# Performance work log

Hardware: AMD Instinct MI355X
Metric: run time of the kernel (lower is better)

## Reference

```python
import jax, jax.numpy as jnp
import numpy as np

B, C, F = 8, 2048, 128


def setup_inputs() -> dict:
    key = jax.random.key(0)
    ks = jax.random.split(key, 13)
    features = jax.random.normal(ks[0], (B, C, F), dtype=jnp.float32)
    # sparse-ish boolean adjacency masks over operations
    pred_mask = jax.random.uniform(ks[1], (B, C, C)) < 0.05
    succ_mask = jax.random.uniform(ks[2], (B, C, C)) < 0.05
    same_type_mask = jax.random.uniform(ks[3], (B, C, C)) < 0.10

    def linear(k, fan_in, fan_out):
        kw, kb = jax.random.split(k)
        bound = 1.0 / np.sqrt(fan_in)
        W = jax.random.uniform(kw, (fan_in, fan_out), minval=-bound, maxval=bound, dtype=jnp.float32)
        b = jax.random.uniform(kb, (fan_out,), minval=-bound, maxval=bound, dtype=jnp.float32)
        return W, b

    W_enc, b_enc = linear(ks[4], F, 4 * F)
    W_space, b_space = linear(ks[5], 3 * F, F)
    W_same, b_same = linear(ks[6], 2 * F, F)
    W_mix, b_mix = linear(ks[7], 2 * F, F)
    return {
        "features": features,
        "pred_mask": pred_mask,
        "succ_mask": succ_mask,
        "same_type_mask": same_type_mask,
        "W_enc": W_enc, "b_enc": b_enc,
        "W_space": W_space, "b_space": b_space,
        "W_same": W_same, "b_same": b_same,
        "W_mix": W_mix, "b_mix": b_mix,
    }


def reference(features, pred_mask, succ_mask, same_type_mask,
              W_enc, b_enc, W_space, b_space, W_same, b_same, W_mix, b_mix):
    # encoder: [B,C,F] -> [B,C,4F], split into origin + 3 message features
    enc = features @ W_enc + b_enc
    origin, e_pred, e_succ, e_same = jnp.split(enc, 4, axis=-1)

    def masked_mean(mask, e):
        # original builds (B,C,C,F) broadcast product then sums over 'other';
        # mathematically this is mask @ e with a clamped-degree divisor.
        m = mask.astype(e.dtype)                         # [B,C,C]
        deg = jnp.maximum(m.sum(-1, keepdims=True), 1.0)  # [B,C,1]
        return jnp.einsum('bij,bjf->bif', m, e) / deg

    pred_f = masked_mean(pred_mask, e_pred)
    succ_f = masked_mean(succ_mask, e_succ)
    same_f = masked_mean(same_type_mask, e_same)

    space_mixed = jnp.concatenate([pred_f, origin, succ_f], axis=-1) @ W_space + b_space
    same_mixed = jnp.concatenate([origin, same_f], axis=-1) @ W_same + b_same
    return jnp.concatenate([space_mixed, same_mixed], axis=-1) @ W_mix + b_mix
```

## Files before the change

kernel.cpp:

```cpp
#include <hip/hip_runtime.h>
#include <stdint.h>

typedef unsigned int uint;
typedef unsigned short ushort;
typedef unsigned char uchar;
typedef __attribute__((ext_vector_type(8))) short bf16x8;
typedef __attribute__((ext_vector_type(4))) float f32x4;

__device__ __forceinline__ ushort f2bf(float f) {
  uint u = __builtin_bit_cast(uint, f);
  return (ushort)((u + 0x7FFFu + ((u >> 16) & 1u)) >> 16);
}

__global__ __launch_bounds__(256) void k_detect(
    const uint* __restrict__ m, int* __restrict__ esz_out) {
  __shared__ int s_ok;
  if (threadIdx.x == 0) s_ok = 1;
  __syncthreads();
  int ok = 1;
  for (int i = 0; i < 64; ++i) {
    uint v = m[(size_t)threadIdx.x * 64 + i];
    if (!(v == 0u || v == 1u || v == 0x3F800000u)) ok = 0;
  }
  if (!ok) atomicAnd(&s_ok, 0);
  __syncthreads();
  if (threadIdx.x == 0) *esz_out = s_ok ? 4 : 1;
}

__global__ __launch_bounds__(256) void k_cvt_feat(
    const float4* __restrict__ in, ushort* __restrict__ out) {
  for (int i = blockIdx.x * 256 + threadIdx.x; i < 524288; i += 65536) {
    float4 v = in[i];
    ushort4 o;
    o.x = f2bf(v.x); o.y = f2bf(v.y); o.z = f2bf(v.z); o.w = f2bf(v.w);
    *(ushort4*)&out[(size_t)i * 4] = o;
  }
}

__global__ __launch_bounds__(256) void k_twt(
    const float* __restrict__ We, const float* __restrict__ Ws,
    const float* __restrict__ Wm, const float* __restrict__ Wx,
    ushort* __restrict__ Te, ushort* __restrict__ Ts,
    ushort* __restrict__ Tm, ushort* __restrict__ Tx) {
  int i = blockIdx.x * 256 + threadIdx.x;
  if (i < 65536) { int n = i >> 7, k = i & 127; Te[i] = f2bf(We[k * 512 + n]); return; }
  i -= 65536;
  if (i < 49152) { int n = i / 384, k = i - n * 384; Ts[i] = f2bf(Ws[k * 128 + n]); return; }
  i -= 49152;
  if (i < 32768) { int n = i >> 8, k = i & 255; Tm[i] = f2bf(Wm[k * 128 + n]); return; }
  i -= 32768;
  if (i < 32768) { int n = i >> 8, k = i & 255; Tx[i] = f2bf(Wx[k * 128 + n]); return; }
}

__device__ __forceinline__ void mfma_tiles(const ushort* As, const ushort* Bs,
                                           int m0w, int n0w, int lr, int quad,
                                           f32x4 acc[2][4]) {
#pragma unroll
  for (int kc = 0; kc < 2; ++kc) {
    bf16x8 a[2], b[4];
#pragma unroll
    for (int i = 0; i < 2; ++i)
      a[i] = *(const bf16x8*)&As[(m0w + i * 16 + lr) * 72 + kc * 32 + quad * 8];
#pragma unroll
    for (int j = 0; j < 4; ++j)
      b[j] = *(const bf16x8*)&Bs[(n0w + j * 16 + lr) * 72 + kc * 32 + quad * 8];
#pragma unroll
    for (int i = 0; i < 2; ++i)
#pragma unroll
      for (int j = 0; j < 4; ++j)
        acc[i][j] = __builtin_amdgcn_mfma_f32_16x16x32_bf16(a[i], b[j], acc[i][j], 0, 0, 0);
  }
}

__global__ __launch_bounds__(256) void k_enc(
    const ushort* __restrict__ featbf, const ushort* __restrict__ WTe,
    const float* __restrict__ bias, ushort* __restrict__ origin,
    ushort* __restrict__ eT0, ushort* __restrict__ eT1, ushort* __restrict__ eT2) {
  __shared__ ushort As[64 * 72];
  __shared__ ushort Bs[128 * 72];
  const int t = threadIdx.x;
  const int gm0 = blockIdx.x * 64;
  const int y = blockIdx.y;
  const ushort* Bsrc = WTe + (size_t)y * 128 * 128;
  const int lane = t & 63, wave = t >> 6;
  const int m0w = (wave >> 1) * 32, n0w = (wave & 1) * 64;
  const int quad = lane >> 4, lr = lane & 15;
  const int am = t >> 2, aq = t & 3;
  const int bn = t >> 1, bh = t & 1;
  f32x4 acc[2][4] = {};
  for (int k0 = 0; k0 < 128; k0 += 64) {
    const ushort* asrc = featbf + (size_t)(gm0 + am) * 128 + k0 + aq * 16;
    bf16x8 av0 = *(const bf16x8*)asrc;
    bf16x8 av1 = *(const bf16x8*)(asrc + 8);
    const ushort* bsrc = Bsrc + (size_t)bn * 128 + k0 + bh * 32;
    bf16x8 bv0 = *(const bf16x8*)bsrc;
    bf16x8 bv1 = *(const bf16x8*)(bsrc + 8);
    bf16x8 bv2 = *(const bf16x8*)(bsrc + 16);
    bf16x8 bv3 = *(const bf16x8*)(bsrc + 24);
    *(bf16x8*)&As[am * 72 + aq * 16] = av0;
    *(bf16x8*)&As[am * 72 + aq * 16 + 8] = av1;
    *(bf16x8*)&Bs[bn * 72 + bh * 32] = bv0;
    *(bf16x8*)&Bs[bn * 72 + bh * 32 + 8] = bv1;
    *(bf16x8*)&Bs[bn * 72 + bh * 32 + 16] = bv2;
    *(bf16x8*)&Bs[bn * 72 + bh * 32 + 24] = bv3;
    __syncthreads();
    mfma_tiles(As, Bs, m0w, n0w, lr, quad, acc);
    __syncthreads();
  }
  ushort* eT = (y == 1) ? eT0 : (y == 2) ? eT1 : eT2;
#pragma unroll
  for (int i = 0; i < 2; ++i)
#pragma unroll
    for (int j = 0; j < 4; ++j)
#pragma unroll
      for (int r = 0; r < 4; ++r) {
        int m = gm0 + m0w + i * 16 + quad * 4 + r;
        int n = n0w + j * 16 + lr;
        ushort h = f2bf(acc[i][j][r] + bias[y * 128 + n]);
        if (y == 0) origin[(size_t)m * 128 + n] = h;
        else eT[(size_t)n * 16384 + m] = h;
      }
}

__global__ __launch_bounds__(256) void k_mm(
    const void* __restrict__ mp, const void* __restrict__ ms, const void* __restrict__ mt,
    const ushort* __restrict__ eT0, const ushort* __restrict__ eT1, const ushort* __restrict__ eT2,
    ushort* __restrict__ P, ushort* __restrict__ S, ushort* __restrict__ T,
    const int* __restrict__ esz_p) {
  __shared__ ushort As[64 * 72];
  __shared__ ushort Bs[128 * 72];
  __shared__ uint degs[64];
  const int t = threadIdx.x;
  const int mtile = blockIdx.x, b = blockIdx.y, mid = blockIdx.z;
  const void* mask = (mid == 0) ? mp : (mid == 1) ? ms : mt;
  const ushort* eT = (mid == 0) ? eT0 : (mid == 1) ? eT1 : eT2;
  ushort* outp = (mid == 0) ? P : (mid == 1) ? S : T;
  const int esz = *esz_p;
  if (t < 64) degs[t] = 0;
  const size_t rowbase = (size_t)b * 2048 + mtile * 64;
  const int lane = t & 63, wave = t >> 6;
  const int m0w = (wave >> 1) * 32, n0w = (wave & 1) * 64;
  const int quad = lane >> 4, lr = lane & 15;
  const int am = t >> 2, aq = t & 3;
  const int bn = t >> 1, bh = t & 1;
  const ushort* bsrc_base = eT + (size_t)bn * 16384 + (size_t)b * 2048 + bh * 32;
  f32x4 acc[2][4] = {};
  int cnt = 0;
  for (int k0 = 0; k0 < 2048; k0 += 64) {
    bf16x8 o0, o1;
    if (esz == 4) {
      const uint* p = (const uint*)mask + (rowbase + am) * 2048 + k0 + aq * 16;
      uint w[16];
      *(uint4*)&w[0] = *(const uint4*)p;
      *(uint4*)&w[4] = *(const uint4*)(p + 4);
      *(uint4*)&w[8] = *(const uint4*)(p + 8);
      *(uint4*)&w[12] = *(const uint4*)(p + 12);
#pragma unroll
      for (int e = 0; e < 8; ++e) { int nz = (w[e] != 0u); o0[e] = nz ? (short)0x3F80 : (short)0; cnt += nz; }
#pragma unroll
      for (int e = 0; e < 8; ++e) { int nz = (w[e + 8] != 0u); o1[e] = nz ? (short)0x3F80 : (short)0; cnt += nz; }
    } else {
      const uchar* p = (const uchar*)mask + (rowbase + am) * 2048 + k0 + aq * 16;
      uint4 wb = *(const uint4*)p;
      uint arr[4] = {wb.x, wb.y, wb.z, wb.w};
#pragma unroll
      for (int e = 0; e < 8; ++e) { int nz = (((arr[e >> 2] >> ((e & 3) * 8)) & 0xFFu) != 0u); o0[e] = nz ? (short)0x3F80 : (short)0; cnt += nz; }
#pragma unroll
      for (int e = 0; e < 8; ++e) { int ee = e + 8; int nz = (((arr[ee >> 2] >> ((ee & 3) * 8)) & 0xFFu) != 0u); o1[e] = nz ? (short)0x3F80 : (short)0; cnt += nz; }
    }
    const ushort* bsrc = bsrc_base + k0;
    bf16x8 bv0 = *(const bf16x8*)bsrc;
    bf16x8 bv1 = *(const bf16x8*)(bsrc + 8);
    bf16x8 bv2 = *(const bf16x8*)(bsrc + 16);
    bf16x8 bv3 = *(const bf16x8*)(bsrc + 24);
    *(bf16x8*)&As[am * 72 + aq * 16] = o0;
    *(bf16x8*)&As[am * 72 + aq * 16 + 8] = o1;
    *(bf16x8*)&Bs[bn * 72 + bh * 32] = bv0;
    *(bf16x8*)&Bs[bn * 72 + bh * 32 + 8] = bv1;
    *(bf16x8*)&Bs[bn * 72 + bh * 32 + 16] = bv2;
    *(bf16x8*)&Bs[bn * 72 + bh * 32 + 24] = bv3;
    __syncthreads();
    mfma_tiles(As, Bs, m0w, n0w, lr, quad, acc);
    __syncthreads();
  }
  atomicAdd(&degs[am], (uint)cnt);
  __syncthreads();
#pragma unroll
  for (int i = 0; i < 2; ++i)
#pragma unroll
    for (int r = 0; r < 4; ++r) {
      int ml = m0w + i * 16 + quad * 4 + r;
      uint d = degs[ml];
      float inv = 1.0f / (float)(d > 0u ? d : 1u);
#pragma unroll
      for (int j = 0; j < 4; ++j) {
        int n = n0w + j * 16 + lr;
        outp[(rowbase + ml) * 128 + n] = f2bf(acc[i][j][r] * inv);
      }
    }
}

__global__ __launch_bounds__(256) void k_gemm(
    const ushort* __restrict__ A0, const ushort* __restrict__ A1,
    const ushort* __restrict__ A2, const ushort* __restrict__ Bsrc,
    int bstride, int K, const float* __restrict__ bias,
    void* __restrict__ out, int out_f32) {
  __shared__ ushort As[64 * 72];
  __shared__ ushort Bs[128 * 72];
  const int t = threadIdx.x;
  const int gm0 = blockIdx.x * 64;
  const int lane = t & 63, wave = t >> 6;
  const int m0w = (wave >> 1) * 32, n0w = (wave & 1) * 64;
  const int quad = lane >> 4, lr = lane & 15;
  const int am = t >> 2, aq = t & 3;
  const int bn = t >> 1, bh = t & 1;
  f32x4 acc[2][4] = {};
  for (int k0 = 0; k0 < K; k0 += 64) {
    const int seg = k0 >> 7;
    const ushort* Ap = (seg == 0) ? A0 : (seg == 1) ? A1 : A2;
    const ushort* asrc = Ap + (size_t)(gm0 + am) * 128 + (k0 & 127) + aq * 16;
    bf16x8 av0 = *(const bf16x8*)asrc;
    bf16x8 av1 = *(const bf16x8*)(asrc + 8);
    const ushort* bsrc = Bsrc + (size_t)bn * bstride + k0 + bh * 32;
    bf16x8 bv0 = *(const bf16x8*)bsrc;
    bf16x8 bv1 = *(const bf16x8*)(bsrc + 8);
    bf16x8 bv2 = *(const bf16x8*)(bsrc + 16);
    bf16x8 bv3 = *(const bf16x8*)(bsrc + 24);
    *(bf16x8*)&As[am * 72 + aq * 16] = av0;
    *(bf16x8*)&As[am * 72 + aq * 16 + 8] = av1;
    *(bf16x8*)&Bs[bn * 72 + bh * 32] = bv0;
    *(bf16x8*)&Bs[bn * 72 + bh * 32 + 8] = bv1;
    *(bf16x8*)&Bs[bn * 72 + bh * 32 + 16] = bv2;
    *(bf16x8*)&Bs[bn * 72 + bh * 32 + 24] = bv3;
    __syncthreads();
    mfma_tiles(As, Bs, m0w, n0w, lr, quad, acc);
    __syncthreads();
  }
#pragma unroll
  for (int i = 0; i < 2; ++i)
#pragma unroll
    for (int j = 0; j < 4; ++j)
#pragma unroll
      for (int r = 0; r < 4; ++r) {
        int m = gm0 + m0w + i * 16 + quad * 4 + r;
        int n = n0w + j * 16 + lr;
        float v = acc[i][j][r] + bias[n];
        if (out_f32) ((float*)out)[(size_t)m * 128 + n] = v;
        else ((ushort*)out)[(size_t)m * 128 + n] = f2bf(v);
      }
}

extern "C" void kernel_launch(void* const* d_in, const int* in_sizes, int n_in,
                              void* d_out, int out_size, void* d_ws,
                              size_t ws_size, hipStream_t stream) {
  const float* features = (const float*)d_in[0];
  const void* pred = d_in[1];
  const void* succ = d_in[2];
  const void* same = d_in[3];
  const float* W_enc = (const float*)d_in[4];
  const float* b_enc = (const float*)d_in[5];
  const float* W_space = (const float*)d_in[6];
  const float* b_space = (const float*)d_in[7];
  const float* W_same = (const float*)d_in[8];
  const float* b_same = (const float*)d_in[9];
  const float* W_mix = (const float*)d_in[10];
  const float* b_mix = (const float*)d_in[11];

  const size_t M = 16384;
  ushort* w = (ushort*)d_ws;
  ushort* feat_bf = w;  w += M * 128;
  ushort* WT_enc = w;   w += 512 * 128;
  ushort* WT_space = w; w += 128 * 384;
  ushort* WT_same = w;  w += 128 * 256;
  ushort* WT_mix = w;   w += 128 * 256;
  ushort* origin = w;   w += M * 128;
  ushort* eT0 = w;      w += M * 128;
  ushort* eT1 = w;      w += M * 128;
  ushort* eT2 = w;      w += M * 128;
  ushort* P = w;        w += M * 128;
  ushort* S = w;        w += M * 128;
  ushort* T = w;        w += M * 128;
  ushort* X = w;        w += M * 128;
  ushort* Y = w;        w += M * 128;
  int* esz = (int*)w;

  k_detect<<<1, 256, 0, stream>>>((const uint*)pred, esz);
  k_cvt_feat<<<256, 256, 0, stream>>>((const float4*)features, feat_bf);
  k_twt<<<704, 256, 0, stream>>>(W_enc, W_space, W_same, W_mix,
                                 WT_enc, WT_space, WT_same, WT_mix);
  k_enc<<<dim3(256, 4), 256, 0, stream>>>(feat_bf, WT_enc, b_enc,
                                          origin, eT0, eT1, eT2);
  k_mm<<<dim3(32, 8, 3), 256, 0, stream>>>(pred, succ, same, eT0, eT1, eT2,
                                           P, S, T, esz);
  k_gemm<<<256, 256, 0, stream>>>(P, origin, S, WT_space, 384, 384,
                                  b_space, X, 0);
  k_gemm<<<256, 256, 0, stream>>>(origin, T, nullptr, WT_same, 256, 256,
                                  b_same, Y, 0);
  k_gemm<<<256, 256, 0, stream>>>(X, Y, nullptr, WT_mix, 256, 256,
                                  b_mix, d_out, 1);
}
```

Baseline: 452.6 us.

## Fold linear layers into encoder weights and fuse mask-matmul with output accumulation

Uses linearity to precompose the space/same/mix weights with the encoder weights on device, so each adjacency term becomes mask @ (features @ U) and the three trailing GEMMs disappear. The per-row bias contributions are folded into constant vectors, applied only when a row's degree is nonzero. The mask kernel now loads masks directly into registers with double buffering instead of staging through LDS, reads pre-swizzled eT tiles written via an LDS stage in the encoder, remaps blocks across XCDs, and accumulates into the fp32 output with atomics. Feature conversion is folded into the encoder and mask-format detection samples across all three masks. The float atomics make the summation order nondeterministic, and composing the weights before rounding to bf16 changes the numerics.

```diff
diff --git a/kernel.cpp b/kernel.cpp
--- a/kernel.cpp
+++ b/kernel.cpp
@@ -13,75 +13,81 @@
 }
 
 __global__ __launch_bounds__(256) void k_detect(
-    const uint* __restrict__ m, int* __restrict__ esz_out) {
-  __shared__ int s_ok;
-  if (threadIdx.x == 0) s_ok = 1;
-  __syncthreads();
-  int ok = 1;
-  for (int i = 0; i < 64; ++i) {
-    uint v = m[(size_t)threadIdx.x * 64 + i];
-    if (!(v == 0u || v == 1u || v == 0x3F800000u)) ok = 0;
-  }
-  if (!ok) atomicAnd(&s_ok, 0);
-  __syncthreads();
-  if (threadIdx.x == 0) *esz_out = s_ok ? 4 : 1;
-}
-
-__global__ __launch_bounds__(256) void k_cvt_feat(
-    const float4* __restrict__ in, ushort* __restrict__ out) {
-  for (int i = blockIdx.x * 256 + threadIdx.x; i < 524288; i += 65536) {
-    float4 v = in[i];
-    ushort4 o;
-    o.x = f2bf(v.x); o.y = f2bf(v.y); o.z = f2bf(v.z); o.w = f2bf(v.w);
-    *(ushort4*)&out[(size_t)i * 4] = o;
-  }
-}
-
-__global__ __launch_bounds__(256) void k_twt(
-    const float* __restrict__ We, const float* __restrict__ Ws,
-    const float* __restrict__ Wm, const float* __restrict__ Wx,
-    ushort* __restrict__ Te, ushort* __restrict__ Ts,
-    ushort* __restrict__ Tm, ushort* __restrict__ Tx) {
-  int i = blockIdx.x * 256 + threadIdx.x;
-  if (i < 65536) { int n = i >> 7, k = i & 127; Te[i] = f2bf(We[k * 512 + n]); return; }
-  i -= 65536;
-  if (i < 49152) { int n = i / 384, k = i - n * 384; Ts[i] = f2bf(Ws[k * 128 + n]); return; }
-  i -= 49152;
-  if (i < 32768) { int n = i >> 8, k = i & 255; Tm[i] = f2bf(Wm[k * 128 + n]); return; }
-  i -= 32768;
-  if (i < 32768) { int n = i >> 8, k = i & 255; Tx[i] = f2bf(Wx[k * 128 + n]); return; }
-}
-
-__device__ __forceinline__ void mfma_tiles(const ushort* As, const ushort* Bs,
-                                           int m0w, int n0w, int lr, int quad,
-                                           f32x4 acc[2][4]) {
-#pragma unroll
-  for (int kc = 0; kc < 2; ++kc) {
-    bf16x8 a[2], b[4];
-#pragma unroll
-    for (int i = 0; i < 2; ++i)
-      a[i] = *(const bf16x8*)&As[(m0w + i * 16 + lr) * 72 + kc * 32 + quad * 8];
-#pragma unroll
-    for (int j = 0; j < 4; ++j)
-      b[j] = *(const bf16x8*)&Bs[(n0w + j * 16 + lr) * 72 + kc * 32 + quad * 8];
-#pragma unroll
-    for (int i = 0; i < 2; ++i)
-#pragma unroll
-      for (int j = 0; j < 4; ++j)
-        acc[i][j] = __builtin_amdgcn_mfma_f32_16x16x32_bf16(a[i], b[j], acc[i][j], 0, 0, 0);
+    const uint* __restrict__ mp, const uint* __restrict__ ms,
+    const uint* __restrict__ mt, int* __restrict__ esz) {
+  int bid = blockIdx.x;
+  const uint* m = (bid < 64) ? mp : (bid < 128) ? ms : mt;
+  uint v = m[(size_t)(bid & 63) * 65521 + threadIdx.x];
+  if (!(v == 0u || v == 1u || v == 0x3F800000u)) atomicAnd(esz, 0);
+}
+
+__global__ __launch_bounds__(256) void k_fuse1(
+    const float* __restrict__ Ws, const float* __restrict__ Wsame,
+    const float* __restrict__ Wm, float* __restrict__ T1, float* __restrict__ T2) {
+  int idx = blockIdx.x * 256 + threadIdx.x;
+  if (idx >= 81920) return;
+  int r = idx >> 7, n = idx & 127;
+  float s = 0.f;
+  if (r < 384) {
+    for (int c = 0; c < 128; ++c) s += Ws[r * 128 + c] * Wm[c * 128 + n];
+    T1[r * 128 + n] = s;
+  } else {
+    int rr = r - 384;
+    for (int c = 0; c < 128; ++c) s += Wsame[rr * 128 + c] * Wm[(128 + c) * 128 + n];
+    T2[rr * 128 + n] = s;
+  }
+}
+
+__global__ __launch_bounds__(256) void k_fuse2(
+    const float* __restrict__ We, const float* __restrict__ be,
+    const float* __restrict__ bs, const float* __restrict__ bsame,
+    const float* __restrict__ bm, const float* __restrict__ Wm,
+    const float* __restrict__ T1, const float* __restrict__ T2,
+    ushort* __restrict__ UT, float* __restrict__ cvec) {
+  int idx = blockIdx.x * 256 + threadIdx.x;
+  if (idx < 65536) {
+    int y = idx >> 14, n = (idx >> 7) & 127, k = idx & 127;
+    float s = 0.f;
+    if (y == 0)
+      for (int m = 0; m < 128; ++m)
+        s += We[k * 512 + m] * (T1[(128 + m) * 128 + n] + T2[m * 128 + n]);
+    else if (y == 1)
+      for (int m = 0; m < 128; ++m) s += We[k * 512 + 128 + m] * T1[m * 128 + n];
+    else if (y == 2)
+      for (int m = 0; m < 128; ++m) s += We[k * 512 + 256 + m] * T1[(256 + m) * 128 + n];
+    else
+      for (int m = 0; m < 128; ++m) s += We[k * 512 + 384 + m] * T2[(128 + m) * 128 + n];
+    UT[((size_t)y * 128 + n) * 128 + k] = f2bf(s);
+  } else if (idx < 66048) {
+    int cid = idx - 65536, cv = cid >> 7, n = cid & 127;
+    float s = 0.f;
+    if (cv == 0) {
+      for (int m = 0; m < 128; ++m)
+        s += be[m] * (T1[(128 + m) * 128 + n] + T2[m * 128 + n]);
+      for (int c = 0; c < 128; ++c) s += bs[c] * Wm[c * 128 + n];
+      for (int c = 0; c < 128; ++c) s += bsame[c] * Wm[(128 + c) * 128 + n];
+      s += bm[n];
+    } else if (cv == 1) {
+      for (int m = 0; m < 128; ++m) s += be[128 + m] * T1[m * 128 + n];
+    } else if (cv == 2) {
+      for (int m = 0; m < 128; ++m) s += be[256 + m] * T1[(256 + m) * 128 + n];
+    } else {
+      for (int m = 0; m < 128; ++m) s += be[384 + m] * T2[(128 + m) * 128 + n];
+    }
+    cvec[cv * 128 + n] = s;
   }
 }
 
 __global__ __launch_bounds__(256) void k_enc(
-    const ushort* __restrict__ featbf, const ushort* __restrict__ WTe,
-    const float* __restrict__ bias, ushort* __restrict__ origin,
+    const float* __restrict__ feat, const ushort* __restrict__ UT,
+    const float* __restrict__ cvec, float* __restrict__ out,
     ushort* __restrict__ eT0, ushort* __restrict__ eT1, ushort* __restrict__ eT2) {
   __shared__ ushort As[64 * 72];
   __shared__ ushort Bs[128 * 72];
+  __shared__ ushort stage[8192];
   const int t = threadIdx.x;
   const int gm0 = blockIdx.x * 64;
   const int y = blockIdx.y;
-  const ushort* Bsrc = WTe + (size_t)y * 128 * 128;
   const int lane = t & 63, wave = t >> 6;
   const int m0w = (wave >> 1) * 32, n0w = (wave & 1) * 64;
   const int quad = lane >> 4, lr = lane & 15;
@@ -89,102 +95,187 @@
   const int bn = t >> 1, bh = t & 1;
   f32x4 acc[2][4] = {};
   for (int k0 = 0; k0 < 128; k0 += 64) {
-    const ushort* asrc = featbf + (size_t)(gm0 + am) * 128 + k0 + aq * 16;
-    bf16x8 av0 = *(const bf16x8*)asrc;
-    bf16x8 av1 = *(const bf16x8*)(asrc + 8);
-    const ushort* bsrc = Bsrc + (size_t)bn * 128 + k0 + bh * 32;
+    const float* asrc = feat + (size_t)(gm0 + am) * 128 + k0 + aq * 16;
+    float4 f0 = *(const float4*)asrc;
+    float4 f1 = *(const float4*)(asrc + 4);
+    float4 f2 = *(const float4*)(asrc + 8);
+    float4 f3 = *(const float4*)(asrc + 12);
+    ushort h[16];
+    h[0] = f2bf(f0.x); h[1] = f2bf(f0.y); h[2] = f2bf(f0.z); h[3] = f2bf(f0.w);
+    h[4] = f2bf(f1.x); h[5] = f2bf(f1.y); h[6] = f2bf(f1.z); h[7] = f2bf(f1.w);
+    h[8] = f2bf(f2.x); h[9] = f2bf(f2.y); h[10] = f2bf(f2.z); h[11] = f2bf(f2.w);
+    h[12] = f2bf(f3.x); h[13] = f2bf(f3.y); h[14] = f2bf(f3.z); h[15] = f2bf(f3.w);
+    const ushort* bsrc = UT + ((size_t)y * 128 + bn) * 128 + k0 + bh * 32;
     bf16x8 bv0 = *(const bf16x8*)bsrc;
     bf16x8 bv1 = *(const bf16x8*)(bsrc + 8);
     bf16x8 bv2 = *(const bf16x8*)(bsrc + 16);
     bf16x8 bv3 = *(const bf16x8*)(bsrc + 24);
-    *(bf16x8*)&As[am * 72 + aq * 16] = av0;
-    *(bf16x8*)&As[am * 72 + aq * 16 + 8] = av1;
+    *(bf16x8*)&As[am * 72 + aq * 16] = *(bf16x8*)&h[0];
+    *(bf16x8*)&As[am * 72 + aq * 16 + 8] = *(bf16x8*)&h[8];
     *(bf16x8*)&Bs[bn * 72 + bh * 32] = bv0;
     *(bf16x8*)&Bs[bn * 72 + bh * 32 + 8] = bv1;
     *(bf16x8*)&Bs[bn * 72 + bh * 32 + 16] = bv2;
     *(bf16x8*)&Bs[bn * 72 + bh * 32 + 24] = bv3;
     __syncthreads();
-    mfma_tiles(As, Bs, m0w, n0w, lr, quad, acc);
+#pragma unroll
+    for (int kc = 0; kc < 2; ++kc) {
+      bf16x8 a[2], b[4];
+#pragma unroll
+      for (int i = 0; i < 2; ++i)
+        a[i] = *(const bf16x8*)&As[(m0w + i * 16 + lr) * 72 + kc * 32 + quad * 8];
+#pragma unroll
+      for (int j = 0; j < 4; ++j)
+        b[j] = *(const bf16x8*)&Bs[(n0w + j * 16 + lr) * 72 + kc * 32 + quad * 8];
+#pragma unroll
+      for (int i = 0; i < 2; ++i)
+#pragma unroll
+        for (int j = 0; j < 4; ++j)
+          acc[i][j] = __builtin_amdgcn_mfma_f32_16x16x32_bf16(a[i], b[j], acc[i][j], 0, 0, 0);
+    }
     __syncthreads();
   }
-  ushort* eT = (y == 1) ? eT0 : (y == 2) ? eT1 : eT2;
-#pragma unroll
-  for (int i = 0; i < 2; ++i)
-#pragma unroll
-    for (int j = 0; j < 4; ++j)
-#pragma unroll
-      for (int r = 0; r < 4; ++r) {
-        int m = gm0 + m0w + i * 16 + quad * 4 + r;
-        int n = n0w + j * 16 + lr;
-        ushort h = f2bf(acc[i][j][r] + bias[y * 128 + n]);
-        if (y == 0) origin[(size_t)m * 128 + n] = h;
-        else eT[(size_t)n * 16384 + m] = h;
-      }
-}
-
-__global__ __launch_bounds__(256) void k_mm(
-    const void* __restrict__ mp, const void* __restrict__ ms, const void* __restrict__ mt,
-    const ushort* __restrict__ eT0, const ushort* __restrict__ eT1, const ushort* __restrict__ eT2,
-    ushort* __restrict__ P, ushort* __restrict__ S, ushort* __restrict__ T,
+  if (y == 0) {
+#pragma unroll
+    for (int i = 0; i < 2; ++i)
+#pragma unroll
+      for (int j = 0; j < 4; ++j)
+#pragma unroll
+        for (int r = 0; r < 4; ++r) {
+          int m = gm0 + m0w + i * 16 + quad * 4 + r;
+          int n = n0w + j * 16 + lr;
+          out[(size_t)m * 128 + n] = acc[i][j][r] + cvec[n];
+        }
+  } else {
+#pragma unroll
+    for (int i = 0; i < 2; ++i)
+#pragma unroll
+      for (int j = 0; j < 4; ++j)
+#pragma unroll
+        for (int r = 0; r < 4; ++r) {
+          int rl = m0w + i * 16 + quad * 4 + r;
+          int n = n0w + j * 16 + lr;
+          int kc = rl >> 5, qd = (rl >> 3) & 3, e = rl & 7;
+          stage[((((n >> 4) * 2 + kc) * 4 + qd) * 16 + (n & 15)) * 8 + e] =
+              f2bf(acc[i][j][r]);
+        }
+    __syncthreads();
+    ushort* eT = (y == 1) ? eT0 : (y == 2) ? eT1 : eT2;
+    ushort* dst = eT + ((size_t)(gm0 >> 11) * 32 + ((gm0 >> 6) & 31)) * 8192 + t * 32;
+    const ushort* src = stage + t * 32;
+#pragma unroll
+    for (int p = 0; p < 4; ++p)
+      *(bf16x8*)(dst + p * 8) = *(const bf16x8*)(src + p * 8);
+  }
+}
+
+__global__ __launch_bounds__(256, 3) void k_mm(
+    const void* __restrict__ mp, const void* __restrict__ ms,
+    const void* __restrict__ mt, const ushort* __restrict__ eT0,
+    const ushort* __restrict__ eT1, const ushort* __restrict__ eT2,
+    const float* __restrict__ cvec, float* __restrict__ out,
     const int* __restrict__ esz_p) {
-  __shared__ ushort As[64 * 72];
-  __shared__ ushort Bs[128 * 72];
   __shared__ uint degs[64];
   const int t = threadIdx.x;
-  const int mtile = blockIdx.x, b = blockIdx.y, mid = blockIdx.z;
+  const int id = blockIdx.x;
+  const int xcd = id & 7, q = id >> 3;
+  const int mtile = q & 31, gg = xcd * 3 + (q >> 5);
+  const int b = gg & 7, mid = gg >> 3;
   const void* mask = (mid == 0) ? mp : (mid == 1) ? ms : mt;
   const ushort* eT = (mid == 0) ? eT0 : (mid == 1) ? eT1 : eT2;
-  ushort* outp = (mid == 0) ? P : (mid == 1) ? S : T;
-  const int esz = *esz_p;
+  const float* cm = cvec + (mid + 1) * 128;
+  const bool is4 = (*esz_p != 0);
   if (t < 64) degs[t] = 0;
-  const size_t rowbase = (size_t)b * 2048 + mtile * 64;
+  __syncthreads();
+
   const int lane = t & 63, wave = t >> 6;
   const int m0w = (wave >> 1) * 32, n0w = (wave & 1) * 64;
   const int quad = lane >> 4, lr = lane & 15;
-  const int am = t >> 2, aq = t & 3;
-  const int bn = t >> 1, bh = t & 1;
-  const ushort* bsrc_base = eT + (size_t)bn * 16384 + (size_t)b * 2048 + bh * 32;
+  const int jb = n0w >> 4;
+  const size_t rowbase = (size_t)b * 2048 + mtile * 64;
+  const size_t r0 = rowbase + m0w + lr;
+  const size_t r1 = r0 + 16;
+  const uint* A40 = (const uint*)mask + r0 * 2048 + quad * 8;
+  const uint* A41 = (const uint*)mask + r1 * 2048 + quad * 8;
+  const uchar* A10 = (const uchar*)mask + r0 * 2048 + quad * 8;
+  const uchar* A11 = (const uchar*)mask + r1 * 2048 + quad * 8;
+  const ushort* bbase = eT + (size_t)b * 32 * 8192 + quad * 128 + lr * 8;
+
   f32x4 acc[2][4] = {};
-  int cnt = 0;
-  for (int k0 = 0; k0 < 2048; k0 += 64) {
-    bf16x8 o0, o1;
-    if (esz == 4) {
-      const uint* p = (const uint*)mask + (rowbase + am) * 2048 + k0 + aq * 16;
-      uint w[16];
-      *(uint4*)&w[0] = *(const uint4*)p;
-      *(uint4*)&w[4] = *(const uint4*)(p + 4);
-      *(uint4*)&w[8] = *(const uint4*)(p + 8);
-      *(uint4*)&w[12] = *(const uint4*)(p + 12);
-#pragma unroll
-      for (int e = 0; e < 8; ++e) { int nz = (w[e] != 0u); o0[e] = nz ? (short)0x3F80 : (short)0; cnt += nz; }
-#pragma unroll
-      for (int e = 0; e < 8; ++e) { int nz = (w[e + 8] != 0u); o1[e] = nz ? (short)0x3F80 : (short)0; cnt += nz; }
+  uint4 pa[2][2][2];
+  uint2 pa8[2][2];
+  bf16x8 pb[2][4];
+  int cnt0 = 0, cnt1 = 0;
+
+#define LOAD_ITER(IT, BUF)                                                   \
+  do {                                                                       \
+    int it_ = (IT);                                                          \
+    if (is4) {                                                               \
+      const uint* p0_ = A40 + it_ * 32;                                      \
+      const uint* p1_ = A41 + it_ * 32;                                      \
+      pa[BUF][0][0] = *(const uint4*)p0_;                                    \
+      pa[BUF][0][1] = *(const uint4*)(p0_ + 4);                              \
+      pa[BUF][1][0] = *(const uint4*)p1_;                                    \
+      pa[BUF][1][1] = *(const uint4*)(p1_ + 4);                              \
+    } else {                                                                 \
+      pa8[BUF][0] = *(const uint2*)(A10 + it_ * 32);                         \
+      pa8[BUF][1] = *(const uint2*)(A11 + it_ * 32);                         \
+    }                                                                        \
+    const ushort* bp_ = bbase + (it_ >> 1) * 8192 + (it_ & 1) * 512;         \
+    _Pragma("unroll")                                                        \
+    for (int j_ = 0; j_ < 4; ++j_)                                           \
+      pb[BUF][j_] = *(const bf16x8*)(bp_ + (jb + j_) * 1024);                \
+  } while (0)
+
+  LOAD_ITER(0, 0);
+#pragma unroll 2
+  for (int it = 0; it < 64; ++it) {
+    const int cur = it & 1;
+    if (it < 63) LOAD_ITER(it + 1, cur ^ 1);
+    union { bf16x8 v; uint u[4]; } af[2];
+    if (is4) {
+#pragma unroll
+      for (int i = 0; i < 2; ++i) {
+        uint x[8] = {pa[cur][i][0].x, pa[cur][i][0].y, pa[cur][i][0].z,
+                     pa[cur][i][0].w, pa[cur][i][1].x, pa[cur][i][1].y,
+                     pa[cur][i][1].z, pa[cur][i][1].w};
+        int c = 0;
+#pragma unroll
+        for (int p = 0; p < 4; ++p) {
+          af[i].u[p] = (x[2 * p] ? 0x3F80u : 0u) | (x[2 * p + 1] ? 0x3F800000u : 0u);
+          c += (x[2 * p] != 0u) + (x[2 * p + 1] != 0u);
+        }
+        if (i == 0) cnt0 += c; else cnt1 += c;
+      }
     } else {
-      const uchar* p = (const uchar*)mask + (rowbase + am) * 2048 + k0 + aq * 16;
-      uint4 wb = *(const uint4*)p;
-      uint arr[4] = {wb.x, wb.y, wb.z, wb.w};
-#pragma unroll
-      for (int e = 0; e < 8; ++e) { int nz = (((arr[e >> 2] >> ((e & 3) * 8)) & 0xFFu) != 0u); o0[e] = nz ? (short)0x3F80 : (short)0; cnt += nz; }
-#pragma unroll
-      for (int e = 0; e < 8; ++e) { int ee = e + 8; int nz = (((arr[ee >> 2] >> ((ee & 3) * 8)) & 0xFFu) != 0u); o1[e] = nz ? (short)0x3F80 : (short)0; cnt += nz; }
+#pragma unroll
+      for (int i = 0; i < 2; ++i) {
+        uint wl = pa8[cur][i].x, wh = pa8[cur][i].y;
+        int c = 0;
+        af[i].u[0] = ((wl & 0xFFu) ? 0x3F80u : 0u) | ((wl & 0xFF00u) ? 0x3F800000u : 0u);
+        af[i].u[1] = ((wl & 0xFF0000u) ? 0x3F80u : 0u) | ((wl & 0xFF000000u) ? 0x3F800000u : 0u);
+        af[i].u[2] = ((wh & 0xFFu) ? 0x3F80u : 0u) | ((wh & 0xFF00u) ? 0x3F800000u : 0u);
+        af[i].u[3] = ((wh & 0xFF0000u) ? 0x3F80u : 0u) | ((wh & 0xFF000000u) ? 0x3F800000u : 0u);
+        c += ((wl & 0xFFu) != 0u) + ((wl & 0xFF00u) != 0u) +
+             ((wl & 0xFF0000u) != 0u) + ((wl & 0xFF000000u) != 0u) +
+             ((wh & 0xFFu) != 0u) + ((wh & 0xFF00u) != 0u) +
+             ((wh & 0xFF0000u) != 0u) + ((wh & 0xFF000000u) != 0u);
+        if (i == 0) cnt0 += c; else cnt1 += c;
+      }
     }
-    const ushort* bsrc = bsrc_base + k0;
-    bf16x8 bv0 = *(const bf16x8*)bsrc;
-    bf16x8 bv1 = *(const bf16x8*)(bsrc + 8);
-    bf16x8 bv2 = *(const bf16x8*)(bsrc + 16);
-    bf16x8 bv3 = *(const bf16x8*)(bsrc + 24);
-    *(bf16x8*)&As[am * 72 + aq * 16] = o0;
-    *(bf16x8*)&As[am * 72 + aq * 16 + 8] = o1;
-    *(bf16x8*)&Bs[bn * 72 + bh * 32] = bv0;
-    *(bf16x8*)&Bs[bn * 72 + bh * 32 + 8] = bv1;
-    *(bf16x8*)&Bs[bn * 72 + bh * 32 + 16] = bv2;
-    *(bf16x8*)&Bs[bn * 72 + bh * 32 + 24] = bv3;
-    __syncthreads();
-    mfma_tiles(As, Bs, m0w, n0w, lr, quad, acc);
-    __syncthreads();
-  }
-  atomicAdd(&degs[am], (uint)cnt);
+#pragma unroll
+    for (int i = 0; i < 2; ++i)
+#pragma unroll
+      for (int j = 0; j < 4; ++j)
+        acc[i][j] = __builtin_amdgcn_mfma_f32_16x16x32_bf16(af[i].v, pb[cur][j], acc[i][j], 0, 0, 0);
+  }
+#undef LOAD_ITER
+
+  if ((wave & 1) == 0) {
+    atomicAdd(&degs[m0w + lr], (uint)cnt0);
+    atomicAdd(&degs[m0w + 16 + lr], (uint)cnt1);
+  }
   __syncthreads();
+
 #pragma unroll
   for (int i = 0; i < 2; ++i)
 #pragma unroll
@@ -192,62 +283,13 @@
       int ml = m0w + i * 16 + quad * 4 + r;
       uint d = degs[ml];
       float inv = 1.0f / (float)(d > 0u ? d : 1u);
+      float ind = (d > 0u) ? 1.0f : 0.0f;
 #pragma unroll
       for (int j = 0; j < 4; ++j) {
         int n = n0w + j * 16 + lr;
-        outp[(rowbase + ml) * 128 + n] = f2bf(acc[i][j][r] * inv);
+        atomicAdd(&out[(rowbase + ml) * 128 + n], acc[i][j][r] * inv + ind * cm[n]);
       }
     }
-}
-
-__global__ __launch_bounds__(256) void k_gemm(
-    const ushort* __restrict__ A0, const ushort* __restrict__ A1,
-    const ushort* __restrict__ A2, const ushort* __restrict__ Bsrc,
-    int bstride, int K, const float* __restrict__ bias,
-    void* __restrict__ out, int out_f32) {
-  __shared__ ushort As[64 * 72];
-  __shared__ ushort Bs[128 * 72];
-  const int t = threadIdx.x;
-  const int gm0 = blockIdx.x * 64;
-  const int lane = t & 63, wave = t >> 6;
-  const int m0w = (wave >> 1) * 32, n0w = (wave & 1) * 64;
-  const int quad = lane >> 4, lr = lane & 15;
-  const int am = t >> 2, aq = t & 3;
-  const int bn = t >> 1, bh = t & 1;
-  f32x4 acc[2][4] = {};
-  for (int k0 = 0; k0 < K; k0 += 64) {
-    const int seg = k0 >> 7;
-    const ushort* Ap = (seg == 0) ? A0 : (seg == 1) ? A1 : A2;
-    const ushort* asrc = Ap + (size_t)(gm0 + am) * 128 + (k0 & 127) + aq * 16;
-    bf16x8 av0 = *(const bf16x8*)asrc;
-    bf16x8 av1 = *(const bf16x8*)(asrc + 8);
-    const ushort* bsrc = Bsrc + (size_t)bn * bstride + k0 + bh * 32;
-    bf16x8 bv0 = *(const bf16x8*)bsrc;
-    bf16x8 bv1 = *(const bf16x8*)(bsrc + 8);
-    bf16x8 bv2 = *(const bf16x8*)(bsrc + 16);
-    bf16x8 bv3 = *(const bf16x8*)(bsrc + 24);
-    *(bf16x8*)&As[am * 72 + aq * 16] = av0;
-    *(bf16x8*)&As[am * 72 + aq * 16 + 8] = av1;
-    *(bf16x8*)&Bs[bn * 72 + bh * 32] = bv0;
-    *(bf16x8*)&Bs[bn * 72 + bh * 32 + 8] = bv1;
-    *(bf16x8*)&Bs[bn * 72 + bh * 32 + 16] = bv2;
-    *(bf16x8*)&Bs[bn * 72 + bh * 32 + 24] = bv3;
-    __syncthreads();
-    mfma_tiles(As, Bs, m0w, n0w, lr, quad, acc);
-    __syncthreads();
-  }
-#pragma unroll
-  for (int i = 0; i < 2; ++i)
-#pragma unroll
-    for (int j = 0; j < 4; ++j)
-#pragma unroll
-      for (int r = 0; r < 4; ++r) {
-        int m = gm0 + m0w + i * 16 + quad * 4 + r;
-        int n = n0w + j * 16 + lr;
-        float v = acc[i][j][r] + bias[n];
-        if (out_f32) ((float*)out)[(size_t)m * 128 + n] = v;
-        else ((ushort*)out)[(size_t)m * 128 + n] = f2bf(v);
-      }
 }
 
 extern "C" void kernel_launch(void* const* d_in, const int* in_sizes, int n_in,
@@ -265,37 +307,24 @@
   const float* b_same = (const float*)d_in[9];
   const float* W_mix = (const float*)d_in[10];
   const float* b_mix = (const float*)d_in[11];
-
-  const size_t M = 16384;
-  ushort* w = (ushort*)d_ws;
-  ushort* feat_bf = w;  w += M * 128;
-  ushort* WT_enc = w;   w += 512 * 128;
-  ushort* WT_space = w; w += 128 * 384;
-  ushort* WT_same = w;  w += 128 * 256;
-  ushort* WT_mix = w;   w += 128 * 256;
-  ushort* origin = w;   w += M * 128;
-  ushort* eT0 = w;      w += M * 128;
-  ushort* eT1 = w;      w += M * 128;
-  ushort* eT2 = w;      w += M * 128;
-  ushort* P = w;        w += M * 128;
-  ushort* S = w;        w += M * 128;
-  ushort* T = w;        w += M * 128;
-  ushort* X = w;        w += M * 128;
-  ushort* Y = w;        w += M * 128;
-  int* esz = (int*)w;
-
-  k_detect<<<1, 256, 0, stream>>>((const uint*)pred, esz);
-  k_cvt_feat<<<256, 256, 0, stream>>>((const float4*)features, feat_bf);
-  k_twt<<<704, 256, 0, stream>>>(W_enc, W_space, W_same, W_mix,
-                                 WT_enc, WT_space, WT_same, WT_mix);
-  k_enc<<<dim3(256, 4), 256, 0, stream>>>(feat_bf, WT_enc, b_enc,
-                                          origin, eT0, eT1, eT2);
-  k_mm<<<dim3(32, 8, 3), 256, 0, stream>>>(pred, succ, same, eT0, eT1, eT2,
-                                           P, S, T, esz);
-  k_gemm<<<256, 256, 0, stream>>>(P, origin, S, WT_space, 384, 384,
-                                  b_space, X, 0);
-  k_gemm<<<256, 256, 0, stream>>>(origin, T, nullptr, WT_same, 256, 256,
-                                  b_same, Y, 0);
-  k_gemm<<<256, 256, 0, stream>>>(X, Y, nullptr, WT_mix, 256, 256,
-                                  b_mix, d_out, 1);
-}
+  float* out = (float*)d_out;
+
+  char* wsb = (char*)d_ws;
+  ushort* UT = (ushort*)wsb;
+  float* cvec = (float*)(wsb + 131072);
+  float* T1 = (float*)(wsb + 133120);
+  float* T2 = (float*)(wsb + 329728);
+  ushort* eT0 = (ushort*)(wsb + 460800);
+  ushort* eT1 = (ushort*)(wsb + 460800 + 4194304);
+  ushort* eT2 = (ushort*)(wsb + 460800 + 8388608);
+  int* esz = (int*)(wsb + 460800 + 12582912);
+
+  hipMemsetAsync(esz, 1, 4, stream);
+  k_detect<<<192, 256, 0, stream>>>((const uint*)pred, (const uint*)succ,
+                                    (const uint*)same, esz);
+  k_fuse1<<<320, 256, 0, stream>>>(W_space, W_same, W_mix, T1, T2);
+  k_fuse2<<<258, 256, 0, stream>>>(W_enc, b_enc, b_space, b_same, b_mix, W_mix,
+                                   T1, T2, UT, cvec);
+  k_enc<<<dim3(256, 4), 256, 0, stream>>>(features, UT, cvec, out, eT0, eT1, eT2);
+  k_mm<<<768, 256, 0, stream>>>(pred, succ, same, eT0, eT1, eT2, cvec, out, esz);
+}
```

After: 470.3 us. 3.9% more time.
